# Optimization experiments

Hardware: AMD Instinct MI355X
Metric: run time of the kernel (lower is better)

The kernel has to match this reference:

```python
import jax, jax.numpy as jnp
import numpy as np

N = 1_000_000  # nodes
E = 1_000_000  # edges (== N so poss_edge can be indexed by node ids AND edge masks, as in source)
C = 64         # classes; poss_edge has C+1 columns (last = 'intrust')
SEMI_LAMBDA = 0.5
EDGE_LAMBDA = 1.0


def setup_inputs() -> dict:
    key = jax.random.key(0)
    k1, k2, k3, k4, k5 = jax.random.split(key, 5)
    # probabilities strictly positive so log() is finite
    poss_node = jax.random.uniform(k1, (N, C), jnp.float32, 0.05, 1.0)
    poss_edge = jax.random.uniform(k2, (E, C + 1), jnp.float32, 0.05, 1.0)
    groundTruth = jax.random.randint(k3, (N,), 0, C)
    mask = jax.random.randint(k4, (N,), 0, 2).astype(bool)
    edges = jax.random.randint(k5, (E, 2), 0, N)
    return {"poss_node": poss_node, "poss_edge": poss_edge,
            "groundTruth": groundTruth, "mask": mask, "edges": edges}


def reference(poss_node, poss_edge, groundTruth, mask, edges):
    dt = poss_node.dtype
    maskf = mask.astype(dt)
    # --- node NLL loss: mean of -log p[i, gt[i]] over masked nodes ---
    logp = jnp.log(poss_node[jnp.arange(N), groundTruth])  # [N]
    loss = -jnp.sum(maskf * logp) / jnp.sum(maskf)

    e0, e1 = edges[:, 0], edges[:, 1]
    intrust = jax.lax.stop_gradient(poss_edge[:, -1])  # detach

    # --- semi loss (faithful to source: scalar sq-diff times sum(1-intrust)) ---
    if SEMI_LAMBDA >= 1e-9:
        sqdiff = jnp.sum((poss_edge[e0] - poss_edge[e1]) ** 2)  # scalar
        semi_loss = SEMI_LAMBDA * jnp.sum(1.0 - intrust) * sqdiff
    else:
        semi_loss = jnp.zeros((), dt)

    # --- edge label splits ---
    m0, m1 = mask[e0], mask[e1]
    label_mask = m0 | m1
    both = m0 & m1
    gt0, gt1 = groundTruth[e0], groundTruth[e1]
    same = both & (gt0 == gt1)
    diff = both & (gt0 != gt1)
    single = label_mask & ~both
    left_s = single & m0
    right_s = single & m1

    rows = jnp.arange(E)
    p_gt0 = poss_edge[rows, gt0]   # [E] prob of left node's label
    p_gt1 = poss_edge[rows, gt1]   # [E] prob of right node's label
    p_last = poss_edge[:, -1]      # [E] 'no-edge' / intrust column

    z = jnp.zeros((), dt)
    raw = (-jnp.sum(jnp.where(same, jnp.log(p_gt0), z))
           - jnp.sum(jnp.where(diff, jnp.log(p_last), z))
           - jnp.sum(jnp.where(left_s, jnp.log(p_last + p_gt0), z))
           - jnp.sum(jnp.where(right_s, jnp.log(p_last + p_gt1), z)))
    S = jnp.sum(label_mask.astype(dt))
    # source applies (*= edge_lambda; /= S) twice
    edge_loss = raw * (EDGE_LAMBDA * EDGE_LAMBDA) / (S * S)

    return loss + semi_loss + edge_loss
```

## Files before the change

kernel.cpp:

```cpp
#include <hip/hip_runtime.h>
#include <math.h>

namespace {
constexpr int N = 1000000;
constexpr int E = 1000000;
constexpr int C = 64;
constexpr int BLOCK = 256;
constexpr int GROUPS_PER_BLOCK = BLOCK / 16;
constexpr int GROUPS8_PER_BLOCK = BLOCK / 8;

constexpr int NODE_BLOCKS = 1024;
constexpr int PREP_BLOCKS = 2048;
constexpr int SQ_BLOCKS   = 2048;
constexpr int PREP_GROUPS = PREP_BLOCKS * GROUPS_PER_BLOCK;
constexpr int SQ_GROUPS   = SQ_BLOCKS * GROUPS8_PER_BLOCK;

constexpr int NODE_BLOCKS_F = 1024;
constexpr int EDGE_BLOCKS_F = 2048;
constexpr int TOTAL_GROUPS_F = EDGE_BLOCKS_F * GROUPS_PER_BLOCK;

constexpr double SEMI_LAMBDA = 0.5;
constexpr double EDGE_LAMBDA = 1.0;

constexpr size_t PE16_ELEMS = (size_t)E * C;
constexpr size_t WS_NEEDED  = PE16_ELEMS * 2
                            + (size_t)E * 4
                            + (size_t)2 * NODE_BLOCKS * 4
                            + (size_t)3 * PREP_BLOCKS * 4
                            + (size_t)1 * SQ_BLOCKS * 4;
}

union H4 { uint2 u2; _Float16 h[4]; };
union H8 { uint4 u4; _Float16 h[8]; };

__device__ __forceinline__ float waveReduceSum(float v) {
#pragma unroll
    for (int off = 32; off > 0; off >>= 1) v += __shfl_down(v, off, 64);
    return v;
}

__device__ __forceinline__ float groupExtract(float c0, float c1, float c2, float c3,
                                              int col, int waveBase) {
    const int slot = col & 3;
    const float lo  = (slot & 1) ? c1 : c0;
    const float hi  = (slot & 1) ? c3 : c2;
    const float sel = (slot & 2) ? hi : lo;
    return __shfl(sel, waveBase + (col >> 2), 64);
}


__global__ __launch_bounds__(BLOCK) void node_kernel(
    const float* __restrict__ poss_node,
    const int* __restrict__ gt,
    const int* __restrict__ mask,
    float* __restrict__ partials)
{
    float lsum = 0.f, cnt = 0.f;
    for (int i = blockIdx.x * BLOCK + threadIdx.x; i < N; i += NODE_BLOCKS * BLOCK) {
        if (mask[i] != 0) {
            lsum += logf(poss_node[(size_t)i * C + gt[i]]);
            cnt += 1.f;
        }
    }
    __shared__ float s0[BLOCK / 64], s1[BLOCK / 64];
    lsum = waveReduceSum(lsum);
    cnt  = waveReduceSum(cnt);
    const int lane = threadIdx.x & 63, wv = threadIdx.x >> 6;
    if (lane == 0) { s0[wv] = lsum; s1[wv] = cnt; }
    __syncthreads();
    if (threadIdx.x == 0) {
        float a = 0.f, b = 0.f;
#pragma unroll
        for (int w = 0; w < BLOCK / 64; ++w) { a += s0[w]; b += s1[w]; }
        partials[blockIdx.x]               = a;
        partials[NODE_BLOCKS + blockIdx.x] = b;
    }
}

__global__ __launch_bounds__(BLOCK) void prep_kernel(
    const float* __restrict__ poss_edge,
    const int* __restrict__ gt,
    const int* __restrict__ mask,
    const int* __restrict__ edges,
    unsigned short* __restrict__ pe16,
    float* __restrict__ plast,
    float* __restrict__ partials)
{
    const int t = threadIdx.x & 15;
    const int g = blockIdx.x * GROUPS_PER_BLOCK + (threadIdx.x >> 4);
    const int waveBase = threadIdx.x & 48;

    float s1 = 0.f, pos = 0.f, lcnt = 0.f;

    for (int r = g; r < E; r += PREP_GROUPS) {
        const float* __restrict__ row = poss_edge + (size_t)r * (C + 1);
        const float c0 = row[4 * t + 0];
        const float c1 = row[4 * t + 1];
        const float c2 = row[4 * t + 2];
        const float c3 = row[4 * t + 3];
        H4 h;
        h.h[0] = (_Float16)c0; h.h[1] = (_Float16)c1;
        h.h[2] = (_Float16)c2; h.h[3] = (_Float16)c3;
        *reinterpret_cast<uint2*>(pe16 + (size_t)r * C + 4 * t) = h.u2;

        const float pl = row[C];
        if (t == 0) {
            plast[r] = pl;
            s1 += 1.f - pl;
        }

        const int2 ep = *(const int2*)(edges + 2 * (size_t)r);
        const int m0 = (mask[ep.x] != 0);
        const int m1 = (mask[ep.y] != 0);
        if (m0 | m1) {
            float contrib;
            if (m0 & m1) {
                const int g0 = gt[ep.x];
                const int g1 = gt[ep.y];
                if (g0 == g1) {
                    contrib = logf(groupExtract(c0, c1, c2, c3, g0, waveBase));
                } else {
                    contrib = logf(pl);
                }
            } else {
                const int gg = m0 ? gt[ep.x] : gt[ep.y];
                contrib = logf(pl + groupExtract(c0, c1, c2, c3, gg, waveBase));
            }
            if (t == 0) { pos += contrib; lcnt += 1.f; }
        }
    }

    __shared__ float s[3][BLOCK / 64];
    s1   = waveReduceSum(s1);
    pos  = waveReduceSum(pos);
    lcnt = waveReduceSum(lcnt);
    const int lane = threadIdx.x & 63, wv = threadIdx.x >> 6;
    if (lane == 0) { s[0][wv] = s1; s[1][wv] = pos; s[2][wv] = lcnt; }
    __syncthreads();
    if (threadIdx.x == 0) {
        float a = 0.f, b = 0.f, c = 0.f;
#pragma unroll
        for (int w = 0; w < BLOCK / 64; ++w) { a += s[0][w]; b += s[1][w]; c += s[2][w]; }
        partials[0 * PREP_BLOCKS + blockIdx.x] = a;
        partials[1 * PREP_BLOCKS + blockIdx.x] = b;
        partials[2 * PREP_BLOCKS + blockIdx.x] = c;
    }
}

__global__ __launch_bounds__(BLOCK) void sq_kernel(
    const unsigned short* __restrict__ pe16,
    const float* __restrict__ plast,
    const int* __restrict__ edges,
    float* __restrict__ partials)
{
    const int t = threadIdx.x & 7;
    const int g = blockIdx.x * GROUPS8_PER_BLOCK + (threadIdx.x >> 3);

    float sq = 0.f;

    for (int e = g; e < E; e += SQ_GROUPS) {
        const int2 ep = *(const int2*)(edges + 2 * (size_t)e);
        H8 ha, hb;
        ha.u4 = *reinterpret_cast<const uint4*>(pe16 + (size_t)ep.x * C + 8 * t);
        hb.u4 = *reinterpret_cast<const uint4*>(pe16 + (size_t)ep.y * C + 8 * t);
        float acc = 0.f;
#pragma unroll
        for (int k = 0; k < 8; ++k) {
            const float d = (float)ha.h[k] - (float)hb.h[k];
            acc = fmaf(d, d, acc);
        }
        if (t == 0) {
            const float dl = plast[ep.x] - plast[ep.y];
            acc = fmaf(dl, dl, acc);
        }
        sq += acc;
    }

    __shared__ float s[BLOCK / 64];
    sq = waveReduceSum(sq);
    const int lane = threadIdx.x & 63, wv = threadIdx.x >> 6;
    if (lane == 0) s[wv] = sq;
    __syncthreads();
    if (threadIdx.x == 0) {
        float a = 0.f;
#pragma unroll
        for (int w = 0; w < BLOCK / 64; ++w) a += s[w];
        partials[blockIdx.x] = a;
    }
}

__global__ __launch_bounds__(BLOCK) void finalize16_kernel(
    const float* __restrict__ node_partials,
    const float* __restrict__ prep_partials,
    const float* __restrict__ sq_partials,
    float* __restrict__ out)
{
    double a0 = 0, a1 = 0, a2 = 0, a3 = 0, a4 = 0, a5 = 0;
    for (int i = threadIdx.x; i < NODE_BLOCKS; i += BLOCK) {
        a0 += (double)node_partials[i];
        a1 += (double)node_partials[NODE_BLOCKS + i];
    }
    for (int i = threadIdx.x; i < PREP_BLOCKS; i += BLOCK) {
        a2 += (double)prep_partials[0 * PREP_BLOCKS + i];
        a3 += (double)prep_partials[1 * PREP_BLOCKS + i];
        a4 += (double)prep_partials[2 * PREP_BLOCKS + i];
    }
    for (int i = threadIdx.x; i < SQ_BLOCKS; i += BLOCK) {
        a5 += (double)sq_partials[i];
    }
#pragma unroll
    for (int off = 32; off > 0; off >>= 1) {
        a0 += __shfl_down(a0, off, 64);
        a1 += __shfl_down(a1, off, 64);
        a2 += __shfl_down(a2, off, 64);
        a3 += __shfl_down(a3, off, 64);
        a4 += __shfl_down(a4, off, 64);
        a5 += __shfl_down(a5, off, 64);
    }
    __shared__ double sd[6][BLOCK / 64];
    const int lane = threadIdx.x & 63, wv = threadIdx.x >> 6;
    if (lane == 0) {
        sd[0][wv] = a0; sd[1][wv] = a1; sd[2][wv] = a2;
        sd[3][wv] = a3; sd[4][wv] = a4; sd[5][wv] = a5;
    }
    __syncthreads();
    if (threadIdx.x == 0) {
        double t[6];
#pragma unroll
        for (int k = 0; k < 6; ++k) {
            double v = 0;
#pragma unroll
            for (int w = 0; w < BLOCK / 64; ++w) v += sd[k][w];
            t[k] = v;
        }
        const double logp_sum  = t[0];
        const double mask_cnt  = t[1];
        const double s1_sum    = t[2];
        const double pos_sum   = t[3];
        const double label_cnt = t[4];
        const double sq_sum    = t[5];

        const double loss      = -logp_sum / mask_cnt;
        const double semi      = SEMI_LAMBDA * s1_sum * sq_sum;
        const double edge_loss = (-pos_sum) * (EDGE_LAMBDA * EDGE_LAMBDA) / (label_cnt * label_cnt);
        out[0] = (float)(loss + semi + edge_loss);
    }
}


__global__ __launch_bounds__(BLOCK) void edge_kernel_f(
    const float* __restrict__ poss_edge,
    const int* __restrict__ gt,
    const int* __restrict__ mask,
    const int* __restrict__ edges,
    float* __restrict__ partials)
{
    const int t   = threadIdx.x & 15;
    const int grp = threadIdx.x >> 4;
    const int globalGroup = blockIdx.x * GROUPS_PER_BLOCK + grp;

    float s1 = 0.f, sq = 0.f, pos = 0.f, lcnt = 0.f;

    for (int e = globalGroup; e < E; e += TOTAL_GROUPS_F) {
        const int2 ep = *(const int2*)(edges + 2 * (size_t)e);
        const int e0 = ep.x, e1 = ep.y;

        const float* __restrict__ ra = poss_edge + (size_t)e0 * (C + 1);
        const float* __restrict__ rb = poss_edge + (size_t)e1 * (C + 1);
        const float* __restrict__ re = poss_edge + (size_t)e  * (C + 1);

        const float a0 = ra[t], a1 = ra[t + 16], a2 = ra[t + 32], a3 = ra[t + 48];
        const float b0 = rb[t], b1 = rb[t + 16], b2 = rb[t + 32], b3 = rb[t + 48];
        const float d0 = a0 - b0, d1 = a1 - b1, d2 = a2 - b2, d3 = a3 - b3;
        float acc = fmaf(d0, d0, fmaf(d1, d1, fmaf(d2, d2, d3 * d3)));
        if (t == 0) {
            const float dl = ra[C] - rb[C];
            acc = fmaf(dl, dl, acc);
        }
        sq += acc;

        const float p_last = re[C];
        const int m0 = (mask[e0] != 0);
        const int m1 = (mask[e1] != 0);
        if (m0 | m1) {
            const int g0 = gt[e0];
            const int g1 = gt[e1];
            float contrib;
            if (m0 & m1) {
                contrib = (g0 == g1) ? logf(re[g0]) : logf(p_last);
            } else if (m0) {
                contrib = logf(p_last + re[g0]);
            } else {
                contrib = logf(p_last + re[g1]);
            }
            if (t == 0) { pos += contrib; lcnt += 1.f; }
        }
        if (t == 0) s1 += 1.f - p_last;
    }

    __shared__ float s[4][BLOCK / 64];
    s1   = waveReduceSum(s1);
    sq   = waveReduceSum(sq);
    pos  = waveReduceSum(pos);
    lcnt = waveReduceSum(lcnt);
    const int lane = threadIdx.x & 63, wv = threadIdx.x >> 6;
    if (lane == 0) { s[0][wv] = s1; s[1][wv] = sq; s[2][wv] = pos; s[3][wv] = lcnt; }
    __syncthreads();
    if (threadIdx.x == 0) {
        float a = 0.f, b = 0.f, c = 0.f, d = 0.f;
#pragma unroll
        for (int w = 0; w < BLOCK / 64; ++w) {
            a += s[0][w]; b += s[1][w]; c += s[2][w]; d += s[3][w];
        }
        partials[0 * EDGE_BLOCKS_F + blockIdx.x] = a;
        partials[1 * EDGE_BLOCKS_F + blockIdx.x] = b;
        partials[2 * EDGE_BLOCKS_F + blockIdx.x] = c;
        partials[3 * EDGE_BLOCKS_F + blockIdx.x] = d;
    }
}

__global__ __launch_bounds__(BLOCK) void finalize_kernel_f(
    const float* __restrict__ node_partials,
    const float* __restrict__ edge_partials,
    float* __restrict__ out)
{
    double a0 = 0, a1 = 0, a2 = 0, a3 = 0, a4 = 0, a5 = 0;
    for (int i = threadIdx.x; i < NODE_BLOCKS_F; i += BLOCK) {
        a0 += (double)node_partials[i];
        a1 += (double)node_partials[NODE_BLOCKS_F + i];
    }
    for (int i = threadIdx.x; i < EDGE_BLOCKS_F; i += BLOCK) {
        a2 += (double)edge_partials[0 * EDGE_BLOCKS_F + i];
        a3 += (double)edge_partials[1 * EDGE_BLOCKS_F + i];
        a4 += (double)edge_partials[2 * EDGE_BLOCKS_F + i];
        a5 += (double)edge_partials[3 * EDGE_BLOCKS_F + i];
    }
#pragma unroll
    for (int off = 32; off > 0; off >>= 1) {
        a0 += __shfl_down(a0, off, 64);
        a1 += __shfl_down(a1, off, 64);
        a2 += __shfl_down(a2, off, 64);
        a3 += __shfl_down(a3, off, 64);
        a4 += __shfl_down(a4, off, 64);
        a5 += __shfl_down(a5, off, 64);
    }
    __shared__ double sd[6][BLOCK / 64];
    const int lane = threadIdx.x & 63, wv = threadIdx.x >> 6;
    if (lane == 0) {
        sd[0][wv] = a0; sd[1][wv] = a1; sd[2][wv] = a2;
        sd[3][wv] = a3; sd[4][wv] = a4; sd[5][wv] = a5;
    }
    __syncthreads();
    if (threadIdx.x == 0) {
        double t[6];
#pragma unroll
        for (int k = 0; k < 6; ++k) {
            double v = 0;
#pragma unroll
            for (int w = 0; w < BLOCK / 64; ++w) v += sd[k][w];
            t[k] = v;
        }
        const double loss      = -t[0] / t[1];
        const double semi      = SEMI_LAMBDA * t[2] * t[3];
        const double edge_loss = (-t[4]) * (EDGE_LAMBDA * EDGE_LAMBDA) / (t[5] * t[5]);
        out[0] = (float)(loss + semi + edge_loss);
    }
}


extern "C" void kernel_launch(void* const* d_in, const int* in_sizes, int n_in,
                              void* d_out, int out_size, void* d_ws, size_t ws_size,
                              hipStream_t stream) {
    const float* poss_node = (const float*)d_in[0];
    const float* poss_edge = (const float*)d_in[1];
    const int*   gt        = (const int*)d_in[2];
    const int*   mask      = (const int*)d_in[3];
    const int*   edges     = (const int*)d_in[4];
    float*       out       = (float*)d_out;

    if (ws_size >= WS_NEEDED) {
        unsigned short* pe16          = (unsigned short*)d_ws;
        float*          plast         = (float*)(pe16 + PE16_ELEMS);
        float*          node_partials = plast + E;
        float*          prep_partials = node_partials + 2 * NODE_BLOCKS;
        float*          sq_partials   = prep_partials + 3 * PREP_BLOCKS;

        node_kernel<<<NODE_BLOCKS, BLOCK, 0, stream>>>(poss_node, gt, mask, node_partials);
        prep_kernel<<<PREP_BLOCKS, BLOCK, 0, stream>>>(
            poss_edge, gt, mask, edges, pe16, plast, prep_partials);
        sq_kernel<<<SQ_BLOCKS, BLOCK, 0, stream>>>(pe16, plast, edges, sq_partials);
        finalize16_kernel<<<1, BLOCK, 0, stream>>>(
            node_partials, prep_partials, sq_partials, out);
    } else {
        float* node_partials = (float*)d_ws;
        float* edge_partials = node_partials + 2 * NODE_BLOCKS_F;

        node_kernel<<<NODE_BLOCKS_F, BLOCK, 0, stream>>>(poss_node, gt, mask, node_partials);
        edge_kernel_f<<<EDGE_BLOCKS_F, BLOCK, 0, stream>>>(poss_edge, gt, mask, edges, edge_partials);
        finalize_kernel_f<<<1, BLOCK, 0, stream>>>(node_partials, edge_partials, out);
    }
}
```

Before: 567.7 us.

## Fuse node-loss blocks into the edge prep kernel and vectorize row loads

Merges the separate node NLL kernel into the edge prep kernel by giving every third block the node-loss work and the other two the row conversion and edge-label work. This removes one kernel launch and lets the node gathers overlap with the edge-row streaming. The per-thread row columns are now read with a single float4 load instead of four scalar loads. Because the row stride is 65 floats, these float4 loads are only 4-byte aligned for most rows, which relies on the hardware tolerating unaligned vector loads.

```diff
diff --git a/kernel.cpp b/kernel.cpp
--- a/kernel.cpp
+++ b/kernel.cpp
@@ -10,9 +10,10 @@
 constexpr int GROUPS8_PER_BLOCK = BLOCK / 8;
 
 constexpr int NODE_BLOCKS = 1024;
-constexpr int PREP_BLOCKS = 2048;
+constexpr int ROWS_BLOCKS = 2048;
+constexpr int FUSED_BLOCKS = 3072;
 constexpr int SQ_BLOCKS   = 2048;
-constexpr int PREP_GROUPS = PREP_BLOCKS * GROUPS_PER_BLOCK;
+constexpr int ROWS_GROUPS = ROWS_BLOCKS * GROUPS_PER_BLOCK;
 constexpr int SQ_GROUPS   = SQ_BLOCKS * GROUPS8_PER_BLOCK;
 
 constexpr int NODE_BLOCKS_F = 1024;
@@ -26,7 +27,7 @@
 constexpr size_t WS_NEEDED  = PE16_ELEMS * 2
                             + (size_t)E * 4
                             + (size_t)2 * NODE_BLOCKS * 4
-                            + (size_t)3 * PREP_BLOCKS * 4
+                            + (size_t)3 * ROWS_BLOCKS * 4
                             + (size_t)1 * SQ_BLOCKS * 4;
 }
 
@@ -49,14 +50,213 @@
 }
 
 
-__global__ __launch_bounds__(BLOCK) void node_kernel(
+__global__ __launch_bounds__(BLOCK) void fused_prep_kernel(
+    const float* __restrict__ poss_node,
+    const float* __restrict__ poss_edge,
+    const int* __restrict__ gt,
+    const int* __restrict__ mask,
+    const int* __restrict__ edges,
+    unsigned short* __restrict__ pe16,
+    float* __restrict__ plast,
+    float* __restrict__ node_partials,
+    float* __restrict__ rows_partials)
+{
+    const int bid = blockIdx.x;
+    const int rem = bid % 3;
+
+    if (rem == 2) {
+        const int node_idx = bid / 3;
+        float lsum = 0.f, cnt = 0.f;
+        for (int i = node_idx * BLOCK + threadIdx.x; i < N; i += NODE_BLOCKS * BLOCK) {
+            if (mask[i] != 0) {
+                lsum += logf(poss_node[(size_t)i * C + gt[i]]);
+                cnt += 1.f;
+            }
+        }
+        __shared__ float s0[BLOCK / 64], s1[BLOCK / 64];
+        lsum = waveReduceSum(lsum);
+        cnt  = waveReduceSum(cnt);
+        const int lane = threadIdx.x & 63, wv = threadIdx.x >> 6;
+        if (lane == 0) { s0[wv] = lsum; s1[wv] = cnt; }
+        __syncthreads();
+        if (threadIdx.x == 0) {
+            float a = 0.f, b = 0.f;
+#pragma unroll
+            for (int w = 0; w < BLOCK / 64; ++w) { a += s0[w]; b += s1[w]; }
+            node_partials[node_idx]               = a;
+            node_partials[NODE_BLOCKS + node_idx] = b;
+        }
+    } else {
+        const int rows_idx = 2 * (bid / 3) + rem;
+        const int t = threadIdx.x & 15;
+        const int g = rows_idx * GROUPS_PER_BLOCK + (threadIdx.x >> 4);
+        const int waveBase = threadIdx.x & 48;
+
+        float s1a = 0.f, pos = 0.f, lcnt = 0.f;
+
+        for (int r = g; r < E; r += ROWS_GROUPS) {
+            const float* __restrict__ row = poss_edge + (size_t)r * (C + 1);
+            const float4 v = *reinterpret_cast<const float4*>(row + 4 * t);
+            const float c0 = v.x, c1 = v.y, c2 = v.z, c3 = v.w;
+            H4 h;
+            h.h[0] = (_Float16)c0; h.h[1] = (_Float16)c1;
+            h.h[2] = (_Float16)c2; h.h[3] = (_Float16)c3;
+            *reinterpret_cast<uint2*>(pe16 + (size_t)r * C + 4 * t) = h.u2;
+
+            const float pl = row[C];
+            if (t == 0) {
+                plast[r] = pl;
+                s1a += 1.f - pl;
+            }
+
+            const int2 ep = *(const int2*)(edges + 2 * (size_t)r);
+            const int m0 = (mask[ep.x] != 0);
+            const int m1 = (mask[ep.y] != 0);
+            if (m0 | m1) {
+                float contrib;
+                if (m0 & m1) {
+                    const int g0 = gt[ep.x];
+                    const int g1 = gt[ep.y];
+                    if (g0 == g1) {
+                        contrib = logf(groupExtract(c0, c1, c2, c3, g0, waveBase));
+                    } else {
+                        contrib = logf(pl);
+                    }
+                } else {
+                    const int gg = m0 ? gt[ep.x] : gt[ep.y];
+                    contrib = logf(pl + groupExtract(c0, c1, c2, c3, gg, waveBase));
+                }
+                if (t == 0) { pos += contrib; lcnt += 1.f; }
+            }
+        }
+
+        __shared__ float s[3][BLOCK / 64];
+        s1a  = waveReduceSum(s1a);
+        pos  = waveReduceSum(pos);
+        lcnt = waveReduceSum(lcnt);
+        const int lane = threadIdx.x & 63, wv = threadIdx.x >> 6;
+        if (lane == 0) { s[0][wv] = s1a; s[1][wv] = pos; s[2][wv] = lcnt; }
+        __syncthreads();
+        if (threadIdx.x == 0) {
+            float a = 0.f, b = 0.f, c = 0.f;
+#pragma unroll
+            for (int w = 0; w < BLOCK / 64; ++w) { a += s[0][w]; b += s[1][w]; c += s[2][w]; }
+            rows_partials[0 * ROWS_BLOCKS + rows_idx] = a;
+            rows_partials[1 * ROWS_BLOCKS + rows_idx] = b;
+            rows_partials[2 * ROWS_BLOCKS + rows_idx] = c;
+        }
+    }
+}
+
+__global__ __launch_bounds__(BLOCK) void sq_kernel(
+    const unsigned short* __restrict__ pe16,
+    const float* __restrict__ plast,
+    const int* __restrict__ edges,
+    float* __restrict__ partials)
+{
+    const int t = threadIdx.x & 7;
+    const int g = blockIdx.x * GROUPS8_PER_BLOCK + (threadIdx.x >> 3);
+
+    float sq = 0.f;
+
+    for (int e = g; e < E; e += SQ_GROUPS) {
+        const int2 ep = *(const int2*)(edges + 2 * (size_t)e);
+        H8 ha, hb;
+        ha.u4 = *reinterpret_cast<const uint4*>(pe16 + (size_t)ep.x * C + 8 * t);
+        hb.u4 = *reinterpret_cast<const uint4*>(pe16 + (size_t)ep.y * C + 8 * t);
+        float acc = 0.f;
+#pragma unroll
+        for (int k = 0; k < 8; ++k) {
+            const float d = (float)ha.h[k] - (float)hb.h[k];
+            acc = fmaf(d, d, acc);
+        }
+        if (t == 0) {
+            const float dl = plast[ep.x] - plast[ep.y];
+            acc = fmaf(dl, dl, acc);
+        }
+        sq += acc;
+    }
+
+    __shared__ float s[BLOCK / 64];
+    sq = waveReduceSum(sq);
+    const int lane = threadIdx.x & 63, wv = threadIdx.x >> 6;
+    if (lane == 0) s[wv] = sq;
+    __syncthreads();
+    if (threadIdx.x == 0) {
+        float a = 0.f;
+#pragma unroll
+        for (int w = 0; w < BLOCK / 64; ++w) a += s[w];
+        partials[blockIdx.x] = a;
+    }
+}
+
+__global__ __launch_bounds__(BLOCK) void finalize16_kernel(
+    const float* __restrict__ node_partials,
+    const float* __restrict__ rows_partials,
+    const float* __restrict__ sq_partials,
+    float* __restrict__ out)
+{
+    double a0 = 0, a1 = 0, a2 = 0, a3 = 0, a4 = 0, a5 = 0;
+    for (int i = threadIdx.x; i < NODE_BLOCKS; i += BLOCK) {
+        a0 += (double)node_partials[i];
+        a1 += (double)node_partials[NODE_BLOCKS + i];
+    }
+    for (int i = threadIdx.x; i < ROWS_BLOCKS; i += BLOCK) {
+        a2 += (double)rows_partials[0 * ROWS_BLOCKS + i];
+        a3 += (double)rows_partials[1 * ROWS_BLOCKS + i];
+        a4 += (double)rows_partials[2 * ROWS_BLOCKS + i];
+    }
+    for (int i = threadIdx.x; i < SQ_BLOCKS; i += BLOCK) {
+        a5 += (double)sq_partials[i];
+    }
+#pragma unroll
+    for (int off = 32; off > 0; off >>= 1) {
+        a0 += __shfl_down(a0, off, 64);
+        a1 += __shfl_down(a1, off, 64);
+        a2 += __shfl_down(a2, off, 64);
+        a3 += __shfl_down(a3, off, 64);
+        a4 += __shfl_down(a4, off, 64);
+        a5 += __shfl_down(a5, off, 64);
+    }
+    __shared__ double sd[6][BLOCK / 64];
+    const int lane = threadIdx.x & 63, wv = threadIdx.x >> 6;
+    if (lane == 0) {
+        sd[0][wv] = a0; sd[1][wv] = a1; sd[2][wv] = a2;
+        sd[3][wv] = a3; sd[4][wv] = a4; sd[5][wv] = a5;
+    }
+    __syncthreads();
+    if (threadIdx.x == 0) {
+        double t[6];
+#pragma unroll
+        for (int k = 0; k < 6; ++k) {
+            double v = 0;
+#pragma unroll
+            for (int w = 0; w < BLOCK / 64; ++w) v += sd[k][w];
+            t[k] = v;
+        }
+        const double logp_sum  = t[0];
+        const double mask_cnt  = t[1];
+        const double s1_sum    = t[2];
+        const double pos_sum   = t[3];
+        const double label_cnt = t[4];
+        const double sq_sum    = t[5];
+
+        const double loss      = -logp_sum / mask_cnt;
+        const double semi      = SEMI_LAMBDA * s1_sum * sq_sum;
+        const double edge_loss = (-pos_sum) * (EDGE_LAMBDA * EDGE_LAMBDA) / (label_cnt * label_cnt);
+        out[0] = (float)(loss + semi + edge_loss);
+    }
+}
+
+
+__global__ __launch_bounds__(BLOCK) void node_kernel_f(
     const float* __restrict__ poss_node,
     const int* __restrict__ gt,
     const int* __restrict__ mask,
     float* __restrict__ partials)
 {
     float lsum = 0.f, cnt = 0.f;
-    for (int i = blockIdx.x * BLOCK + threadIdx.x; i < N; i += NODE_BLOCKS * BLOCK) {
+    for (int i = blockIdx.x * BLOCK + threadIdx.x; i < N; i += NODE_BLOCKS_F * BLOCK) {
         if (mask[i] != 0) {
             lsum += logf(poss_node[(size_t)i * C + gt[i]]);
             cnt += 1.f;
@@ -72,181 +272,10 @@
         float a = 0.f, b = 0.f;
 #pragma unroll
         for (int w = 0; w < BLOCK / 64; ++w) { a += s0[w]; b += s1[w]; }
-        partials[blockIdx.x]               = a;
-        partials[NODE_BLOCKS + blockIdx.x] = b;
-    }
-}
-
-__global__ __launch_bounds__(BLOCK) void prep_kernel(
-    const float* __restrict__ poss_edge,
-    const int* __restrict__ gt,
-    const int* __restrict__ mask,
-    const int* __restrict__ edges,
-    unsigned short* __restrict__ pe16,
-    float* __restrict__ plast,
-    float* __restrict__ partials)
-{
-    const int t = threadIdx.x & 15;
-    const int g = blockIdx.x * GROUPS_PER_BLOCK + (threadIdx.x >> 4);
-    const int waveBase = threadIdx.x & 48;
-
-    float s1 = 0.f, pos = 0.f, lcnt = 0.f;
-
-    for (int r = g; r < E; r += PREP_GROUPS) {
-        const float* __restrict__ row = poss_edge + (size_t)r * (C + 1);
-        const float c0 = row[4 * t + 0];
-        const float c1 = row[4 * t + 1];
-        const float c2 = row[4 * t + 2];
-        const float c3 = row[4 * t + 3];
-        H4 h;
-        h.h[0] = (_Float16)c0; h.h[1] = (_Float16)c1;
-        h.h[2] = (_Float16)c2; h.h[3] = (_Float16)c3;
-        *reinterpret_cast<uint2*>(pe16 + (size_t)r * C + 4 * t) = h.u2;
-
-        const float pl = row[C];
-        if (t == 0) {
-            plast[r] = pl;
-            s1 += 1.f - pl;
-        }
-
-        const int2 ep = *(const int2*)(edges + 2 * (size_t)r);
-        const int m0 = (mask[ep.x] != 0);
-        const int m1 = (mask[ep.y] != 0);
-        if (m0 | m1) {
-            float contrib;
-            if (m0 & m1) {
-                const int g0 = gt[ep.x];
-                const int g1 = gt[ep.y];
-                if (g0 == g1) {
-                    contrib = logf(groupExtract(c0, c1, c2, c3, g0, waveBase));
-                } else {
-                    contrib = logf(pl);
-                }
-            } else {
-                const int gg = m0 ? gt[ep.x] : gt[ep.y];
-                contrib = logf(pl + groupExtract(c0, c1, c2, c3, gg, waveBase));
-            }
-            if (t == 0) { pos += contrib; lcnt += 1.f; }
-        }
-    }
-
-    __shared__ float s[3][BLOCK / 64];
-    s1   = waveReduceSum(s1);
-    pos  = waveReduceSum(pos);
-    lcnt = waveReduceSum(lcnt);
-    const int lane = threadIdx.x & 63, wv = threadIdx.x >> 6;
-    if (lane == 0) { s[0][wv] = s1; s[1][wv] = pos; s[2][wv] = lcnt; }
-    __syncthreads();
-    if (threadIdx.x == 0) {
-        float a = 0.f, b = 0.f, c = 0.f;
-#pragma unroll
-        for (int w = 0; w < BLOCK / 64; ++w) { a += s[0][w]; b += s[1][w]; c += s[2][w]; }
-        partials[0 * PREP_BLOCKS + blockIdx.x] = a;
-        partials[1 * PREP_BLOCKS + blockIdx.x] = b;
-        partials[2 * PREP_BLOCKS + blockIdx.x] = c;
-    }
-}
-
-__global__ __launch_bounds__(BLOCK) void sq_kernel(
-    const unsigned short* __restrict__ pe16,
-    const float* __restrict__ plast,
-    const int* __restrict__ edges,
-    float* __restrict__ partials)
-{
-    const int t = threadIdx.x & 7;
-    const int g = blockIdx.x * GROUPS8_PER_BLOCK + (threadIdx.x >> 3);
-
-    float sq = 0.f;
-
-    for (int e = g; e < E; e += SQ_GROUPS) {
-        const int2 ep = *(const int2*)(edges + 2 * (size_t)e);
-        H8 ha, hb;
-        ha.u4 = *reinterpret_cast<const uint4*>(pe16 + (size_t)ep.x * C + 8 * t);
-        hb.u4 = *reinterpret_cast<const uint4*>(pe16 + (size_t)ep.y * C + 8 * t);
-        float acc = 0.f;
-#pragma unroll
-        for (int k = 0; k < 8; ++k) {
-            const float d = (float)ha.h[k] - (float)hb.h[k];
-            acc = fmaf(d, d, acc);
-        }
-        if (t == 0) {
-            const float dl = plast[ep.x] - plast[ep.y];
-            acc = fmaf(dl, dl, acc);
-        }
-        sq += acc;
-    }
-
-    __shared__ float s[BLOCK / 64];
-    sq = waveReduceSum(sq);
-    const int lane = threadIdx.x & 63, wv = threadIdx.x >> 6;
-    if (lane == 0) s[wv] = sq;
-    __syncthreads();
-    if (threadIdx.x == 0) {
-        float a = 0.f;
-#pragma unroll
-        for (int w = 0; w < BLOCK / 64; ++w) a += s[w];
-        partials[blockIdx.x] = a;
-    }
-}
-
-__global__ __launch_bounds__(BLOCK) void finalize16_kernel(
-    const float* __restrict__ node_partials,
-    const float* __restrict__ prep_partials,
-    const float* __restrict__ sq_partials,
-    float* __restrict__ out)
-{
-    double a0 = 0, a1 = 0, a2 = 0, a3 = 0, a4 = 0, a5 = 0;
-    for (int i = threadIdx.x; i < NODE_BLOCKS; i += BLOCK) {
-        a0 += (double)node_partials[i];
-        a1 += (double)node_partials[NODE_BLOCKS + i];
-    }
-    for (int i = threadIdx.x; i < PREP_BLOCKS; i += BLOCK) {
-        a2 += (double)prep_partials[0 * PREP_BLOCKS + i];
-        a3 += (double)prep_partials[1 * PREP_BLOCKS + i];
-        a4 += (double)prep_partials[2 * PREP_BLOCKS + i];
-    }
-    for (int i = threadIdx.x; i < SQ_BLOCKS; i += BLOCK) {
-        a5 += (double)sq_partials[i];
-    }
-#pragma unroll
-    for (int off = 32; off > 0; off >>= 1) {
-        a0 += __shfl_down(a0, off, 64);
-        a1 += __shfl_down(a1, off, 64);
-        a2 += __shfl_down(a2, off, 64);
-        a3 += __shfl_down(a3, off, 64);
-        a4 += __shfl_down(a4, off, 64);
-        a5 += __shfl_down(a5, off, 64);
-    }
-    __shared__ double sd[6][BLOCK / 64];
-    const int lane = threadIdx.x & 63, wv = threadIdx.x >> 6;
-    if (lane == 0) {
-        sd[0][wv] = a0; sd[1][wv] = a1; sd[2][wv] = a2;
-        sd[3][wv] = a3; sd[4][wv] = a4; sd[5][wv] = a5;
-    }
-    __syncthreads();
-    if (threadIdx.x == 0) {
-        double t[6];
-#pragma unroll
-        for (int k = 0; k < 6; ++k) {
-            double v = 0;
-#pragma unroll
-            for (int w = 0; w < BLOCK / 64; ++w) v += sd[k][w];
-            t[k] = v;
-        }
-        const double logp_sum  = t[0];
-        const double mask_cnt  = t[1];
-        const double s1_sum    = t[2];
-        const double pos_sum   = t[3];
-        const double label_cnt = t[4];
-        const double sq_sum    = t[5];
-
-        const double loss      = -logp_sum / mask_cnt;
-        const double semi      = SEMI_LAMBDA * s1_sum * sq_sum;
-        const double edge_loss = (-pos_sum) * (EDGE_LAMBDA * EDGE_LAMBDA) / (label_cnt * label_cnt);
-        out[0] = (float)(loss + semi + edge_loss);
-    }
-}
-
+        partials[blockIdx.x]                 = a;
+        partials[NODE_BLOCKS_F + blockIdx.x] = b;
+    }
+}
 
 __global__ __launch_bounds__(BLOCK) void edge_kernel_f(
     const float* __restrict__ poss_edge,
@@ -382,20 +411,20 @@
         unsigned short* pe16          = (unsigned short*)d_ws;
         float*          plast         = (float*)(pe16 + PE16_ELEMS);
         float*          node_partials = plast + E;
-        float*          prep_partials = node_partials + 2 * NODE_BLOCKS;
-        float*          sq_partials   = prep_partials + 3 * PREP_BLOCKS;
-
-        node_kernel<<<NODE_BLOCKS, BLOCK, 0, stream>>>(poss_node, gt, mask, node_partials);
-        prep_kernel<<<PREP_BLOCKS, BLOCK, 0, stream>>>(
-            poss_edge, gt, mask, edges, pe16, plast, prep_partials);
+        float*          rows_partials = node_partials + 2 * NODE_BLOCKS;
+        float*          sq_partials   = rows_partials + 3 * ROWS_BLOCKS;
+
+        fused_prep_kernel<<<FUSED_BLOCKS, BLOCK, 0, stream>>>(
+            poss_node, poss_edge, gt, mask, edges, pe16, plast,
+            node_partials, rows_partials);
         sq_kernel<<<SQ_BLOCKS, BLOCK, 0, stream>>>(pe16, plast, edges, sq_partials);
         finalize16_kernel<<<1, BLOCK, 0, stream>>>(
-            node_partials, prep_partials, sq_partials, out);
+            node_partials, rows_partials, sq_partials, out);
     } else {
         float* node_partials = (float*)d_ws;
         float* edge_partials = node_partials + 2 * NODE_BLOCKS_F;
 
-        node_kernel<<<NODE_BLOCKS_F, BLOCK, 0, stream>>>(poss_node, gt, mask, node_partials);
+        node_kernel_f<<<NODE_BLOCKS_F, BLOCK, 0, stream>>>(poss_node, gt, mask, node_partials);
         edge_kernel_f<<<EDGE_BLOCKS_F, BLOCK, 0, stream>>>(poss_edge, gt, mask, edges, edge_partials);
         finalize_kernel_f<<<1, BLOCK, 0, stream>>>(node_partials, edge_partials, out);
     }
```

After: 606.2 us. 6.8% more time.
